# Kernel optimization log

Hardware: AMD Instinct MI355X
Metric: run time of the kernel (lower is better)

Reference implementation:

```python
import jax, jax.numpy as jnp
import numpy as np

IN_FEATURES = 4096
OUT_FEATURES = 8192
PADDED = 8192  # 2**ceil(log2(out_features))


def fwht(x):
    """Fast Walsh-Hadamard transform over last axis (n power of 2), normalized by 1/sqrt(n)."""
    orig_shape = x.shape
    n = orig_shape[-1]
    h = x.reshape(-1, n)
    step = 1
    while step < n:  # static loop, log2(n) iterations
        h = h.reshape(-1, n // (2 * step), 2, step)
        a = h[:, :, 0, :]
        b = h[:, :, 1, :]
        h = jnp.stack([a + b, a - b], axis=2).reshape(-1, n)
        step *= 2
    return (h * (1.0 / np.sqrt(n)).astype(np.float32)).reshape(orig_shape)


def setup_inputs() -> dict:
    key = jax.random.key(0)
    kx, kb, kg, kp = jax.random.split(key, 4)
    x = jax.random.normal(kx, (8192, IN_FEATURES), dtype=jnp.float32)
    B = jnp.where(jax.random.uniform(kb, (PADDED,)) < 0.5, -1.0, 1.0).astype(jnp.float32)
    G = jax.random.normal(kg, (PADDED,), dtype=jnp.float32)
    perm = jax.random.permutation(kp, PADDED).astype(jnp.int32)
    return {"x": x, "B": B, "G": G, "perm": perm}


def reference(x, B, G, perm):
    lead = x.shape[:-1]
    flat = x.reshape(-1, IN_FEATURES)
    pad_len = PADDED - IN_FEATURES
    if pad_len > 0:
        flat = jnp.pad(flat, ((0, 0), (0, pad_len)))
    out = flat * B[None, :]
    out = fwht(out)
    out = out[:, perm]
    out = out * G[None, :]
    out = fwht(out)
    out = out[:, :OUT_FEATURES]
    return out.reshape(*lead, OUT_FEATURES)
```

## Files before the change

### kernel.cpp

```cpp
#include <hip/hip_runtime.h>


constexpr int N  = 8192;
constexpr int NT = 256;
constexpr int NR = 32;
constexpr int LDS_WORDS = N + 2 * (N / 32);

__device__ __forceinline__ int padw(int w) { return w + 2 * (w >> 5); }

template <int FIRST_MASK>
__device__ __forceinline__ void butterfly(float v[NR]) {
    #pragma unroll
    for (int b = FIRST_MASK; b < NR; b <<= 1) {
        #pragma unroll
        for (int r = 0; r < NR; ++r) {
            if ((r & b) == 0) {
                float a = v[r], c = v[r ^ b];
                v[r]     = a + c;
                v[r ^ b] = a - c;
            }
        }
    }
}

__global__ __launch_bounds__(NT, 4) void fastfood_kernel(
    const float* __restrict__ x, const float* __restrict__ Bv,
    const float* __restrict__ Gv, const int* __restrict__ perm,
    float* __restrict__ out)
{
    __shared__ float lds[LDS_WORDS];
    const int t = threadIdx.x;
    const int row = blockIdx.x;
    const float* xrow = x + (size_t)row * 4096;

    const int wA = 2 * t;
    const int wB = t * 32;
    const int wC = (t >> 4) * 512 + (t & 15) * 2;

    float v[NR];

    #pragma unroll
    for (int m = 0; m < 8; ++m) {
        int j = m * 512 + wA;
        float2 xv = *(const float2*)(xrow + j);
        float2 bv = *(const float2*)(Bv + j);
        v[2 * m]     = xv.x * bv.x;
        v[2 * m + 1] = xv.y * bv.y;
    }
    #pragma unroll
    for (int m = 8; m < 16; ++m) { v[2 * m] = 0.f; v[2 * m + 1] = 0.f; }

    butterfly<1>(v);
    #pragma unroll
    for (int m = 0; m < 16; ++m)
        *(float2*)&lds[padw(m * 512 + wA)] = make_float2(v[2 * m], v[2 * m + 1]);
    __syncthreads();

    #pragma unroll
    for (int m = 0; m < 16; ++m) {
        float2 d = *(const float2*)&lds[padw(wB + 2 * m)];
        v[2 * m] = d.x; v[2 * m + 1] = d.y;
    }
    butterfly<2>(v);
    #pragma unroll
    for (int m = 0; m < 16; ++m)
        *(float2*)&lds[padw(wB + 2 * m)] = make_float2(v[2 * m], v[2 * m + 1]);
    __syncthreads();

    #pragma unroll
    for (int m = 0; m < 16; ++m) {
        float2 d = *(const float2*)&lds[padw(wC + m * 32)];
        v[2 * m] = d.x; v[2 * m + 1] = d.y;
    }
    int2 q[16];
    #pragma unroll
    for (int m = 0; m < 16; ++m)
        q[m] = *(const int2*)(perm + wC + m * 32);
    butterfly<2>(v);
    #pragma unroll
    for (int m = 0; m < 16; ++m)
        *(float2*)&lds[padw(wC + m * 32)] = make_float2(v[2 * m], v[2 * m + 1]);
    __syncthreads();

    #pragma unroll
    for (int m = 0; m < 16; ++m) {
        float2 g = *(const float2*)(Gv + wC + m * 32);
        v[2 * m]     = lds[q[m].x + 2 * (q[m].x >> 5)] * g.x;
        v[2 * m + 1] = lds[q[m].y + 2 * (q[m].y >> 5)] * g.y;
    }

    butterfly<1>(v);
    __syncthreads();
    #pragma unroll
    for (int m = 0; m < 16; ++m)
        *(float2*)&lds[padw(wC + m * 32)] = make_float2(v[2 * m], v[2 * m + 1]);
    __syncthreads();

    #pragma unroll
    for (int m = 0; m < 16; ++m) {
        float2 d = *(const float2*)&lds[padw(wB + 2 * m)];
        v[2 * m] = d.x; v[2 * m + 1] = d.y;
    }
    butterfly<2>(v);
    #pragma unroll
    for (int m = 0; m < 16; ++m)
        *(float2*)&lds[padw(wB + 2 * m)] = make_float2(v[2 * m], v[2 * m + 1]);
    __syncthreads();

    #pragma unroll
    for (int m = 0; m < 16; ++m) {
        float2 d = *(const float2*)&lds[padw(m * 512 + wA)];
        v[2 * m] = d.x; v[2 * m + 1] = d.y;
    }
    butterfly<2>(v);

    const float scale = 1.0f / 8192.0f;
    float* orow = out + (size_t)row * 8192;
    #pragma unroll
    for (int m = 0; m < 16; ++m) {
        int j = m * 512 + wA;
        *(float2*)(orow + j) = make_float2(v[2 * m] * scale, v[2 * m + 1] * scale);
    }
}

extern "C" void kernel_launch(void* const* d_in, const int* in_sizes, int n_in,
                              void* d_out, int out_size, void* d_ws, size_t ws_size,
                              hipStream_t stream) {
    const float* x    = (const float*)d_in[0];
    const float* Bv   = (const float*)d_in[1];
    const float* Gv   = (const float*)d_in[2];
    const int*   perm = (const int*)d_in[3];
    float* out = (float*)d_out;
    fastfood_kernel<<<dim3(8192), dim3(NT), 0, stream>>>(x, Bv, Gv, perm, out);
}
```

Baseline: 377.9 us.

## Process each row with one 64-lane wave holding 128 values per lane

Result: slower. 420.3 us (+11.2%).

```diff
diff --git a/kernel.cpp b/kernel.cpp
--- a/kernel.cpp
+++ b/kernel.cpp
@@ -1,19 +1,20 @@
 #include <hip/hip_runtime.h>
 
 
-constexpr int N  = 8192;
-constexpr int NT = 256;
-constexpr int NR = 32;
-constexpr int LDS_WORDS = N + 2 * (N / 32);
+constexpr int NT = 64;
+constexpr int LDS_WORDS = 8192 + 256;
 
-__device__ __forceinline__ int padw(int w) { return w + 2 * (w >> 5); }
+using f4 = __attribute__((ext_vector_type(4))) float;
+using i4 = __attribute__((ext_vector_type(4))) int;
 
-template <int FIRST_MASK>
-__device__ __forceinline__ void butterfly(float v[NR]) {
+__device__ __forceinline__ int padw(int w) { return w + ((w >> 7) << 2); }
+
+template <int FIRST>
+__device__ __forceinline__ void bfly(float (&v)[128]) {
     #pragma unroll
-    for (int b = FIRST_MASK; b < NR; b <<= 1) {
+    for (int b = FIRST; b < 128; b <<= 1) {
         #pragma unroll
-        for (int r = 0; r < NR; ++r) {
+        for (int r = 0; r < 128; ++r) {
             if ((r & b) == 0) {
                 float a = v[r], c = v[r ^ b];
                 v[r]     = a + c;
@@ -23,104 +24,96 @@
     }
 }
 
-__global__ __launch_bounds__(NT, 4) void fastfood_kernel(
+__device__ __forceinline__ void bfly_lane1(float (&v)[128], float sgn) {
+    #pragma unroll
+    for (int r = 0; r < 128; ++r) {
+        int t = __builtin_amdgcn_update_dpp(0, __float_as_int(v[r]),
+                                            0xB1 ,
+                                            0xF, 0xF, true);
+        v[r] = fmaf(v[r], sgn, __int_as_float(t));
+    }
+}
+
+__global__ __launch_bounds__(NT, 1) void fastfood_kernel(
     const float* __restrict__ x, const float* __restrict__ Bv,
     const float* __restrict__ Gv, const int* __restrict__ perm,
     float* __restrict__ out)
 {
     __shared__ float lds[LDS_WORDS];
-    const int t = threadIdx.x;
+    const int l = threadIdx.x;
     const int row = blockIdx.x;
     const float* xrow = x + (size_t)row * 4096;
+    float v[128];
 
-    const int wA = 2 * t;
-    const int wB = t * 32;
-    const int wC = (t >> 4) * 512 + (t & 15) * 2;
-
-    float v[NR];
-
-    #pragma unroll
-    for (int m = 0; m < 8; ++m) {
-        int j = m * 512 + wA;
-        float2 xv = *(const float2*)(xrow + j);
-        float2 bv = *(const float2*)(Bv + j);
-        v[2 * m]     = xv.x * bv.x;
-        v[2 * m + 1] = xv.y * bv.y;
-    }
-    #pragma unroll
-    for (int m = 8; m < 16; ++m) { v[2 * m] = 0.f; v[2 * m + 1] = 0.f; }
-
-    butterfly<1>(v);
-    #pragma unroll
-    for (int m = 0; m < 16; ++m)
-        *(float2*)&lds[padw(m * 512 + wA)] = make_float2(v[2 * m], v[2 * m + 1]);
-    __syncthreads();
+    const float scale = 1.0f / 8192.0f;
 
     #pragma unroll
     for (int m = 0; m < 16; ++m) {
-        float2 d = *(const float2*)&lds[padw(wB + 2 * m)];
-        v[2 * m] = d.x; v[2 * m + 1] = d.y;
+        f4 xv = __builtin_nontemporal_load((const f4*)(xrow + m * 256 + 4 * l));
+        f4 bv = *(const f4*)(Bv + m * 256 + 4 * l);
+        v[4 * m + 0] = xv.x * (bv.x * scale);
+        v[4 * m + 1] = xv.y * (bv.y * scale);
+        v[4 * m + 2] = xv.z * (bv.z * scale);
+        v[4 * m + 3] = xv.w * (bv.w * scale);
     }
-    butterfly<2>(v);
     #pragma unroll
-    for (int m = 0; m < 16; ++m)
-        *(float2*)&lds[padw(wB + 2 * m)] = make_float2(v[2 * m], v[2 * m + 1]);
+    for (int r = 64; r < 128; ++r) v[r] = 0.0f;
+
+    bfly<1>(v);
+
+    const int wL0 = 4 * l + 4 * (l >> 5);
+    const int wL1 = 132 * l;
+    #pragma unroll
+    for (int m = 0; m < 32; ++m)
+        *(f4*)&lds[m * 264 + wL0] = f4{v[4 * m], v[4 * m + 1], v[4 * m + 2], v[4 * m + 3]};
+    __syncthreads();
+    #pragma unroll
+    for (int m = 0; m < 32; ++m) {
+        f4 d = *(const f4*)&lds[wL1 + 4 * m];
+        v[4 * m] = d.x; v[4 * m + 1] = d.y; v[4 * m + 2] = d.z; v[4 * m + 3] = d.w;
+    }
+
+    bfly<4>(v);
+    const float sgn = (l & 1) ? -1.0f : 1.0f;
+    bfly_lane1(v, sgn);
+
+    #pragma unroll
+    for (int m = 0; m < 32; ++m)
+        *(f4*)&lds[wL1 + 4 * m] = f4{v[4 * m], v[4 * m + 1], v[4 * m + 2], v[4 * m + 3]};
     __syncthreads();
 
+    const int jbase = 128 * l;
     #pragma unroll
-    for (int m = 0; m < 16; ++m) {
-        float2 d = *(const float2*)&lds[padw(wC + m * 32)];
-        v[2 * m] = d.x; v[2 * m + 1] = d.y;
+    for (int m = 0; m < 32; ++m) {
+        i4 q = *(const i4*)(perm + jbase + 4 * m);
+        f4 g = *(const f4*)(Gv + jbase + 4 * m);
+        v[4 * m + 0] = lds[padw(q.x)] * g.x;
+        v[4 * m + 1] = lds[padw(q.y)] * g.y;
+        v[4 * m + 2] = lds[padw(q.z)] * g.z;
+        v[4 * m + 3] = lds[padw(q.w)] * g.w;
     }
-    int2 q[16];
-    #pragma unroll
-    for (int m = 0; m < 16; ++m)
-        q[m] = *(const int2*)(perm + wC + m * 32);
-    butterfly<2>(v);
-    #pragma unroll
-    for (int m = 0; m < 16; ++m)
-        *(float2*)&lds[padw(wC + m * 32)] = make_float2(v[2 * m], v[2 * m + 1]);
-    __syncthreads();
+
+    bfly<1>(v);
+    bfly_lane1(v, sgn);
 
     #pragma unroll
-    for (int m = 0; m < 16; ++m) {
-        float2 g = *(const float2*)(Gv + wC + m * 32);
-        v[2 * m]     = lds[q[m].x + 2 * (q[m].x >> 5)] * g.x;
-        v[2 * m + 1] = lds[q[m].y + 2 * (q[m].y >> 5)] * g.y;
+    for (int m = 0; m < 32; ++m)
+        *(f4*)&lds[wL1 + 4 * m] = f4{v[4 * m], v[4 * m + 1], v[4 * m + 2], v[4 * m + 3]};
+    __syncthreads();
+    #pragma unroll
+    for (int m = 0; m < 32; ++m) {
+        f4 d = *(const f4*)&lds[m * 264 + wL0];
+        v[4 * m] = d.x; v[4 * m + 1] = d.y; v[4 * m + 2] = d.z; v[4 * m + 3] = d.w;
     }
 
-    butterfly<1>(v);
-    __syncthreads();
-    #pragma unroll
-    for (int m = 0; m < 16; ++m)
-        *(float2*)&lds[padw(wC + m * 32)] = make_float2(v[2 * m], v[2 * m + 1]);
-    __syncthreads();
+    bfly<4>(v);
 
-    #pragma unroll
-    for (int m = 0; m < 16; ++m) {
-        float2 d = *(const float2*)&lds[padw(wB + 2 * m)];
-        v[2 * m] = d.x; v[2 * m + 1] = d.y;
-    }
-    butterfly<2>(v);
-    #pragma unroll
-    for (int m = 0; m < 16; ++m)
-        *(float2*)&lds[padw(wB + 2 * m)] = make_float2(v[2 * m], v[2 * m + 1]);
-    __syncthreads();
-
-    #pragma unroll
-    for (int m = 0; m < 16; ++m) {
-        float2 d = *(const float2*)&lds[padw(m * 512 + wA)];
-        v[2 * m] = d.x; v[2 * m + 1] = d.y;
-    }
-    butterfly<2>(v);
-
-    const float scale = 1.0f / 8192.0f;
     float* orow = out + (size_t)row * 8192;
     #pragma unroll
-    for (int m = 0; m < 16; ++m) {
-        int j = m * 512 + wA;
-        *(float2*)(orow + j) = make_float2(v[2 * m] * scale, v[2 * m + 1] * scale);
-    }
+    for (int m = 0; m < 32; ++m)
+        __builtin_nontemporal_store(
+            f4{v[4 * m], v[4 * m + 1], v[4 * m + 2], v[4 * m + 3]},
+            (f4*)(orow + m * 256 + 4 * l));
 }
 
 extern "C" void kernel_launch(void* const* d_in, const int* in_sizes, int n_in,
```
